# Kernel optimization log

Measured on AMD Instinct MI355X. Metric: run time of the kernel, lower is better.

Reference implementation:

```python
import jax, jax.numpy as jnp
import numpy as np

B, C, P1, P2, H, W = 4096, 64, 2, 2, 11, 5
DIM = H * W          # 55
NHD = 8 * (DIM // 8) # 48 = n_head * d (heads never split in original)
SCALE = 1.0 / np.sqrt(np.float32(NHD))


def _rearrange1(x):
    # b c (p1 h) (p2 w) -> (b c) (p1 p2) (h w)
    x = x.reshape(B, C, P1, H, P2, W)
    x = x.transpose(0, 1, 2, 4, 3, 5)  # b c p1 p2 h w
    return x.reshape(B * C, P1 * P2, H * W)


def _rearrange2(y):
    # (b c) (p1 p2) (h w) -> b c (p1 h) (p2 w)
    y = y.reshape(B, C, P1, P2, H, W)
    y = y.transpose(0, 1, 2, 4, 3, 5)  # b c p1 h p2 w
    return y.reshape(B, C, P1 * H, P2 * W)


def setup_inputs() -> dict:
    key = jax.random.key(0)
    ks = jax.random.split(key, 6)
    std = 1.0 / np.sqrt(np.float32(DIM))
    x = jax.random.normal(ks[0], (B, C, P1 * H, P2 * W), dtype=jnp.float32)
    w_q = jax.random.normal(ks[1], (NHD, DIM), dtype=jnp.float32) * std
    w_k = jax.random.normal(ks[2], (NHD, DIM), dtype=jnp.float32) * std
    w_v = jax.random.normal(ks[3], (NHD, DIM), dtype=jnp.float32) * std
    w_fc = jax.random.normal(ks[4], (DIM, NHD), dtype=jnp.float32) * std
    b_fc = jnp.zeros((DIM,), dtype=jnp.float32)
    return {"x": x, "w_q": w_q, "w_k": w_k, "w_v": w_v, "w_fc": w_fc, "b_fc": b_fc}


def reference(x, w_q, w_k, w_v, w_fc, b_fc):
    xr = _rearrange1(x)                                  # (B*C, 4, 55)
    q = jnp.einsum('nsd,ed->nse', xr, w_q)               # (B*C, 4, 48)
    k = jnp.einsum('nsd,ed->nse', xr, w_k)
    v = jnp.einsum('nsd,ed->nse', xr, w_v)
    attn = jnp.einsum('nse,nte->nst', q, k) * SCALE      # (B*C, 4, 4)
    attn = jax.nn.softmax(attn, axis=-1)
    a = jnp.einsum('nst,nte->nse', attn, v)              # (B*C, 4, 48)
    out = jnp.einsum('nse,de->nsd', a, w_fc) + b_fc      # (B*C, 4, 55)
    return _rearrange2(out)                              # (B, C, 22, 10)
```

## Files before the change

### kernel.cpp

```cpp
#include <hip/hip_runtime.h>


#define QB(v, ctrl) __int_as_float(__builtin_amdgcn_update_dpp( \
    0, __float_as_int(v), (ctrl), 0xf, 0xf, true))

#define PAD 56

__global__ void setup_weights(const float* __restrict__ wq,
                              const float* __restrict__ wk,
                              const float* __restrict__ wv,
                              const float* __restrict__ wfc,
                              const float* __restrict__ bfc,
                              float* __restrict__ ws) {
    int i = blockIdx.x * blockDim.x + threadIdx.x;
    if (i < 55 * PAD) {
        int dp = i / PAD, d = i % PAD;
        if (d < 55) {
            float m1 = 0.f, p = 0.f;
            for (int e = 0; e < 48; ++e) {
                m1 += wq[e * 55 + d] * wk[e * 55 + dp];
                p  += wv[e * 55 + d] * wfc[dp * 48 + e];
            }
            ws[dp * PAD + d]            = m1 * 0.14433756729740643f;
            ws[55 * PAD + dp * PAD + d] = p;
        } else {
            ws[dp * PAD + d]            = 0.f;
            ws[55 * PAD + dp * PAD + d] = 0.f;
        }
    }
    if (i < 55) ws[110 * PAD + i] = bfc[i];
}

__global__ void __launch_bounds__(128)
attn_main(const float* __restrict__ x,
          const float* __restrict__ ws,
          float* __restrict__ out) {
    __shared__ __align__(16) float lds[32 * 220];
    const float* __restrict__ M1T = ws;
    const float* __restrict__ PT  = ws + 55 * PAD;
    const float* __restrict__ BS  = ws + 110 * PAD;

    const int tid = threadIdx.x;
    const size_t seq0 = (size_t)blockIdx.x * 32;
    const float* __restrict__ xb = x + seq0 * 220;
    float* __restrict__ ob = out + seq0 * 220;

    {
        const uint4* __restrict__ src = (const uint4*)xb;
        uint4* dst = (uint4*)lds;
        #pragma unroll
        for (int it = 0; it < 14; ++it) {
            int i = tid + it * 128;
            if (i < 1760) dst[i] = src[i];
        }
    }
    __syncthreads();

    const int t      = tid & 3;
    const int sl     = tid >> 2;
    const int tokoff = (t >> 1) * 110 + (t & 1) * 5;
    const int base   = sl * 220 + tokoff;

    float xreg[PAD];
    #pragma unroll
    for (int d = 0; d < 55; ++d) {
        const int doff = (d / 5) * 10 + (d % 5);
        xreg[d] = lds[base + doff];
    }
    xreg[55] = 0.f;

    float la0 = 0.f, la1 = 0.f, la2 = 0.f, la3 = 0.f;
    for (int h = 0; h < 11; ++h) {
        float xc[5];
        #pragma unroll
        for (int w = 0; w < 5; ++w) xc[w] = lds[base + h * 10 + w];

        #pragma unroll
        for (int w = 0; w < 5; ++w) {
            const int dp = h * 5 + w;
            const float4* __restrict__ m4 = (const float4*)(M1T + dp * PAD);
            float a0 = 0.f, a1 = 0.f, a2 = 0.f, a3 = 0.f;
            #pragma unroll
            for (int d4 = 0; d4 < 14; ++d4) {
                const float4 mm = m4[d4];
                a0 = fmaf(xreg[4 * d4 + 0], mm.x, a0);
                a1 = fmaf(xreg[4 * d4 + 1], mm.y, a1);
                a2 = fmaf(xreg[4 * d4 + 2], mm.z, a2);
                a3 = fmaf(xreg[4 * d4 + 3], mm.w, a3);
            }
            const float t1 = (a0 + a1) + (a2 + a3);
            la0 = fmaf(t1, QB(xc[w], 0x00), la0);
            la1 = fmaf(t1, QB(xc[w], 0x55), la1);
            la2 = fmaf(t1, QB(xc[w], 0xAA), la2);
            la3 = fmaf(t1, QB(xc[w], 0xFF), la3);
        }
    }

    const float mx = fmaxf(fmaxf(la0, la1), fmaxf(la2, la3));
    const float e0 = __expf(la0 - mx), e1 = __expf(la1 - mx);
    const float e2 = __expf(la2 - mx), e3 = __expf(la3 - mx);
    const float inv = 1.0f / (e0 + e1 + e2 + e3);
    const float p0 = e0 * inv, p1 = e1 * inv, p2 = e2 * inv, p3 = e3 * inv;

    __syncthreads();

    for (int h = 0; h < 11; ++h) {
        #pragma unroll
        for (int w = 0; w < 5; ++w) {
            const int dp = h * 5 + w;
            const float4* __restrict__ pc4 = (const float4*)(PT + dp * PAD);
            float a0 = 0.f, a1 = 0.f, a2 = 0.f, a3 = 0.f;
            #pragma unroll
            for (int d4 = 0; d4 < 14; ++d4) {
                const float4 mm = pc4[d4];
                a0 = fmaf(xreg[4 * d4 + 0], mm.x, a0);
                a1 = fmaf(xreg[4 * d4 + 1], mm.y, a1);
                a2 = fmaf(xreg[4 * d4 + 2], mm.z, a2);
                a3 = fmaf(xreg[4 * d4 + 3], mm.w, a3);
            }
            const float t2 = (a0 + a1) + (a2 + a3);
            float o = BS[dp];
            o = fmaf(p0, QB(t2, 0x00), o);
            o = fmaf(p1, QB(t2, 0x55), o);
            o = fmaf(p2, QB(t2, 0xAA), o);
            o = fmaf(p3, QB(t2, 0xFF), o);
            lds[base + h * 10 + w] = o;
        }
    }
    __syncthreads();

    {
        const uint4* __restrict__ src = (const uint4*)lds;
        uint4* dst = (uint4*)ob;
        #pragma unroll
        for (int it = 0; it < 14; ++it) {
            int i = tid + it * 128;
            if (i < 1760) dst[i] = src[i];
        }
    }
}

extern "C" void kernel_launch(void* const* d_in, const int* in_sizes, int n_in,
                              void* d_out, int out_size, void* d_ws, size_t ws_size,
                              hipStream_t stream) {
    const float* x   = (const float*)d_in[0];
    const float* wq  = (const float*)d_in[1];
    const float* wk  = (const float*)d_in[2];
    const float* wv  = (const float*)d_in[3];
    const float* wfc = (const float*)d_in[4];
    const float* bfc = (const float*)d_in[5];
    float* ws = (float*)d_ws;

    const int nseq = out_size / 220;
    const int nblk = nseq / 32;

    hipLaunchKernelGGL(setup_weights, dim3(13), dim3(256), 0, stream,
                       wq, wk, wv, wfc, bfc, ws);
    hipLaunchKernelGGL(attn_main, dim3(nblk), dim3(128), 0, stream,
                       x, ws, (float*)d_out);
}
```

Measured before the change: 752.4 us.

## Drop LDS staging and load/store tokens directly from global memory

Removes the shared-memory staging buffer and block-wide syncs. Each thread now reads its token's 55 values straight from global memory using unaligned 4-wide loads plus a scalar, and writes its outputs the same way. Block size doubles to 256 threads (64 sequences per block). The intent is to free LDS, cut the barriers and the extra copy, and raise occupancy. The cost is less coalesced, unaligned global accesses, since each thread touches strided 5-float chunks, which relies on the cache to absorb the inefficiency.

```diff
diff --git a/kernel.cpp b/kernel.cpp
--- a/kernel.cpp
+++ b/kernel.cpp
@@ -5,6 +5,9 @@
     0, __float_as_int(v), (ctrl), 0xf, 0xf, true))
 
 #define PAD 56
+
+typedef float vf4 __attribute__((ext_vector_type(4)));
+typedef float uvf4 __attribute__((ext_vector_type(4), aligned(4)));
 
 __global__ void setup_weights(const float* __restrict__ wq,
                               const float* __restrict__ wk,
@@ -31,58 +34,47 @@
     if (i < 55) ws[110 * PAD + i] = bfc[i];
 }
 
-__global__ void __launch_bounds__(128)
+__global__ void __launch_bounds__(256)
 attn_main(const float* __restrict__ x,
           const float* __restrict__ ws,
           float* __restrict__ out) {
-    __shared__ __align__(16) float lds[32 * 220];
     const float* __restrict__ M1T = ws;
     const float* __restrict__ PT  = ws + 55 * PAD;
     const float* __restrict__ BS  = ws + 110 * PAD;
 
     const int tid = threadIdx.x;
-    const size_t seq0 = (size_t)blockIdx.x * 32;
-    const float* __restrict__ xb = x + seq0 * 220;
-    float* __restrict__ ob = out + seq0 * 220;
-
-    {
-        const uint4* __restrict__ src = (const uint4*)xb;
-        uint4* dst = (uint4*)lds;
-        #pragma unroll
-        for (int it = 0; it < 14; ++it) {
-            int i = tid + it * 128;
-            if (i < 1760) dst[i] = src[i];
-        }
-    }
-    __syncthreads();
-
-    const int t      = tid & 3;
-    const int sl     = tid >> 2;
+    const int t   = tid & 3;
+    const size_t sq = ((size_t)blockIdx.x * 256 + tid) >> 2;
     const int tokoff = (t >> 1) * 110 + (t & 1) * 5;
-    const int base   = sl * 220 + tokoff;
+    const float* __restrict__ xt = x   + sq * 220 + tokoff;
+    float* __restrict__ ot       = out + sq * 220 + tokoff;
 
     float xreg[PAD];
     #pragma unroll
-    for (int d = 0; d < 55; ++d) {
-        const int doff = (d / 5) * 10 + (d % 5);
-        xreg[d] = lds[base + doff];
+    for (int h = 0; h < 11; ++h) {
+        const uvf4 v = *(const uvf4*)(xt + h * 10);
+        xreg[5 * h + 0] = v.x;
+        xreg[5 * h + 1] = v.y;
+        xreg[5 * h + 2] = v.z;
+        xreg[5 * h + 3] = v.w;
+        xreg[5 * h + 4] = xt[h * 10 + 4];
     }
     xreg[55] = 0.f;
 
     float la0 = 0.f, la1 = 0.f, la2 = 0.f, la3 = 0.f;
     for (int h = 0; h < 11; ++h) {
-        float xc[5];
-        #pragma unroll
-        for (int w = 0; w < 5; ++w) xc[w] = lds[base + h * 10 + w];
+        const uvf4 c4 = *(const uvf4*)(xt + h * 10);
+        const float c5 = xt[h * 10 + 4];
+        const float xc[5] = {c4.x, c4.y, c4.z, c4.w, c5};
 
         #pragma unroll
         for (int w = 0; w < 5; ++w) {
             const int dp = h * 5 + w;
-            const float4* __restrict__ m4 = (const float4*)(M1T + dp * PAD);
+            const vf4* __restrict__ m4 = (const vf4*)(M1T + dp * PAD);
             float a0 = 0.f, a1 = 0.f, a2 = 0.f, a3 = 0.f;
             #pragma unroll
             for (int d4 = 0; d4 < 14; ++d4) {
-                const float4 mm = m4[d4];
+                const vf4 mm = m4[d4];
                 a0 = fmaf(xreg[4 * d4 + 0], mm.x, a0);
                 a1 = fmaf(xreg[4 * d4 + 1], mm.y, a1);
                 a2 = fmaf(xreg[4 * d4 + 2], mm.z, a2);
@@ -102,41 +94,33 @@
     const float inv = 1.0f / (e0 + e1 + e2 + e3);
     const float p0 = e0 * inv, p1 = e1 * inv, p2 = e2 * inv, p3 = e3 * inv;
 
-    __syncthreads();
-
     for (int h = 0; h < 11; ++h) {
+        float o[5];
         #pragma unroll
         for (int w = 0; w < 5; ++w) {
             const int dp = h * 5 + w;
-            const float4* __restrict__ pc4 = (const float4*)(PT + dp * PAD);
+            const vf4* __restrict__ pc4 = (const vf4*)(PT + dp * PAD);
             float a0 = 0.f, a1 = 0.f, a2 = 0.f, a3 = 0.f;
             #pragma unroll
             for (int d4 = 0; d4 < 14; ++d4) {
-                const float4 mm = pc4[d4];
+                const vf4 mm = pc4[d4];
                 a0 = fmaf(xreg[4 * d4 + 0], mm.x, a0);
                 a1 = fmaf(xreg[4 * d4 + 1], mm.y, a1);
                 a2 = fmaf(xreg[4 * d4 + 2], mm.z, a2);
                 a3 = fmaf(xreg[4 * d4 + 3], mm.w, a3);
             }
             const float t2 = (a0 + a1) + (a2 + a3);
-            float o = BS[dp];
-            o = fmaf(p0, QB(t2, 0x00), o);
-            o = fmaf(p1, QB(t2, 0x55), o);
-            o = fmaf(p2, QB(t2, 0xAA), o);
-            o = fmaf(p3, QB(t2, 0xFF), o);
-            lds[base + h * 10 + w] = o;
+            float oo = BS[dp];
+            oo = fmaf(p0, QB(t2, 0x00), oo);
+            oo = fmaf(p1, QB(t2, 0x55), oo);
+            oo = fmaf(p2, QB(t2, 0xAA), oo);
+            oo = fmaf(p3, QB(t2, 0xFF), oo);
+            o[w] = oo;
         }
-    }
-    __syncthreads();
-
-    {
-        const uint4* __restrict__ src = (const uint4*)lds;
-        uint4* dst = (uint4*)ob;
-        #pragma unroll
-        for (int it = 0; it < 14; ++it) {
-            int i = tid + it * 128;
-            if (i < 1760) dst[i] = src[i];
-        }
+        uvf4 st;
+        st.x = o[0]; st.y = o[1]; st.z = o[2]; st.w = o[3];
+        *(uvf4*)(ot + h * 10) = st;
+        ot[h * 10 + 4] = o[4];
     }
 }
 
@@ -152,10 +136,10 @@
     float* ws = (float*)d_ws;
 
     const int nseq = out_size / 220;
-    const int nblk = nseq / 32;
+    const int nblk = nseq / 64;
 
     hipLaunchKernelGGL(setup_weights, dim3(13), dim3(256), 0, stream,
                        wq, wk, wv, wfc, bfc, ws);
-    hipLaunchKernelGGL(attn_main, dim3(nblk), dim3(128), 0, stream,
+    hipLaunchKernelGGL(attn_main, dim3(nblk), dim3(256), 0, stream,
                        x, ws, (float*)d_out);
 }
```

After: 719.7 us. 1.05x faster.
